# Performance work log

Measured on AMD Instinct MI355X. Metric: run time of the kernel, lower is better.

The kernel has to match this reference:

```python
import jax, jax.numpy as jnp
import numpy as np

B, S = 64, 512
VOCAB, DIM, FFDIM, NHEADS, BLOCKS = 512, 128, 512, 4, 4
MASK_INTER_CHOICES = False
LN_EPS = 1e-5
NEG = -1e30


def setup_inputs() -> dict:
    key = jax.random.key(0)
    ks = jax.random.split(key, 12)
    s = 0.02
    inp = dict(
        token_idxes=jax.random.randint(ks[0], (B, S), 0, VOCAB),
        n_pad_lefts=jax.random.randint(ks[1], (B,), 0, 9),
        cards_picked_n=jax.random.randint(ks[2], (B,), 1, 4),
        cards_skipped_n=jax.random.randint(ks[3], (B,), 1, 4),
        n_upgrades=jax.random.randint(ks[4], (B, S), 0, 3),
        emb=jax.random.normal(ks[5], (VOCAB, DIM), jnp.float32) * s,
        in_proj_w=jax.random.normal(ks[6], (BLOCKS, 3 * DIM, DIM), jnp.float32) * s,
        in_proj_b=jnp.zeros((BLOCKS, 3 * DIM), jnp.float32),
        out_w=jax.random.normal(ks[7], (BLOCKS, DIM, DIM), jnp.float32) * s,
        out_b=jnp.zeros((BLOCKS, DIM), jnp.float32),
        ln1_g=jnp.ones((BLOCKS, DIM), jnp.float32),
        ln1_b=jnp.zeros((BLOCKS, DIM), jnp.float32),
        ff1_w=jax.random.normal(ks[8], (BLOCKS, FFDIM, DIM), jnp.float32) * s,
        ff1_b=jnp.zeros((BLOCKS, FFDIM), jnp.float32),
        ff2_w=jax.random.normal(ks[9], (BLOCKS, DIM, FFDIM), jnp.float32) * s,
        ff2_b=jnp.zeros((BLOCKS, DIM), jnp.float32),
        ln2_g=jnp.ones((BLOCKS, DIM), jnp.float32),
        ln2_b=jnp.zeros((BLOCKS, DIM), jnp.float32),
        proj_w=jax.random.normal(ks[10], (2, DIM), jnp.float32) * s,
        proj_b=jnp.zeros((2,), jnp.float32),
    )
    return inp


def build_allowed(n_pad, n_choice):
    # allowed[b, i, j] == True where attention is permitted (torch mask==0)
    pos = jnp.arange(S)
    i = pos[None, :, None]
    j = pos[None, None, :]
    npd = n_pad[:, None, None]
    nc = n_choice[:, None, None]
    mid_i = (i >= npd) & (i < S - nc)
    mid_j = (j >= npd) & (j < S - nc)
    ch_i = i >= S - nc
    ch_j = j >= S - nc
    allowed = ((i < npd) & (i == j)) | (mid_i & mid_j) | (ch_i & mid_j)
    if MASK_INTER_CHOICES:
        allowed = allowed | (ch_i & (i == j))
    else:
        allowed = allowed | (ch_i & ch_j)
    return allowed  # [B, S, S]


def layernorm(x, g, b):
    m = jnp.mean(x, axis=-1, keepdims=True)
    v = jnp.var(x, axis=-1, keepdims=True)
    return (x - m) / jnp.sqrt(v + LN_EPS) * g + b


def mha_block(x, allowed, w_in, b_in, w_out, b_out, g1, b1, w1, bf1, w2, bf2, g2, b2):
    hd = DIM // NHEADS
    qkv = x @ w_in.T + b_in                       # [B,S,3D]
    q, k, v = jnp.split(qkv, 3, axis=-1)
    def heads(t):
        return t.reshape(x.shape[0], S, NHEADS, hd).transpose(0, 2, 1, 3)
    q, k, v = heads(q), heads(k), heads(v)
    scores = jnp.einsum('bhqd,bhkd->bhqk', q, k) / np.float32(np.sqrt(hd))
    scores = jnp.where(allowed[:, None, :, :], scores, NEG)
    attn = jax.nn.softmax(scores, axis=-1)
    o = jnp.einsum('bhqk,bhkd->bhqd', attn, v)
    o = o.transpose(0, 2, 1, 3).reshape(x.shape[0], S, DIM)
    o = o @ w_out.T + b_out
    x = layernorm(x + o, g1, b1)
    ff = jax.nn.relu(x @ w1.T + bf1) @ w2.T + bf2
    return layernorm(x + ff, g2, b2)


def reference(token_idxes, n_pad_lefts, cards_picked_n, cards_skipped_n, n_upgrades,
              emb, in_proj_w, in_proj_b, out_w, out_b, ln1_g, ln1_b,
              ff1_w, ff1_b, ff2_w, ff2_b, ln2_g, ln2_b, proj_w, proj_b):
    n_choice = cards_picked_n + cards_skipped_n
    feat = emb[token_idxes]                                   # [B,S,D]
    pos = jnp.arange(S)
    ch0 = (pos[None, :] >= n_choice[:, None]).astype(feat.dtype)
    feat = feat.at[:, :, 0].set(ch0)
    feat = feat.at[:, :, 1].set(jnp.clip(n_upgrades, 0, 1).astype(feat.dtype))
    allowed = build_allowed(n_pad_lefts, n_choice)
    for l in range(BLOCKS):
        feat = mha_block(feat, allowed, in_proj_w[l], in_proj_b[l], out_w[l], out_b[l],
                         ln1_g[l], ln1_b[l], ff1_w[l], ff1_b[l], ff2_w[l], ff2_b[l],
                         ln2_g[l], ln2_b[l])
    logits = feat @ proj_w.T + proj_b                          # [B,S,2]
    return jax.nn.softmax(logits, axis=2)
```

## Files before the change

kernel.cpp:

```cpp
#include <hip/hip_runtime.h>

#define CB   64
#define CS   512
#define CD   128
#define CH   4
#define CFF  512
#define CL   4
#define NEG_BIG -3.0e38f
#define SCALE 0.17677669529663687f
#define EXSC  0.25505654050961364f

typedef __attribute__((ext_vector_type(8))) short short8;
typedef __attribute__((ext_vector_type(4))) float f32x4;
typedef __attribute__((ext_vector_type(4))) unsigned int u32x4;

static __device__ __forceinline__ unsigned short f2b(float f) {
  union { float f; unsigned int u; } v; v.f = f;
  unsigned int u = v.u;
  unsigned int r = (u + 0x7fffu + ((u >> 16) & 1u)) >> 16;
  return (unsigned short)r;
}

__global__ void k_cvt_all(const float* __restrict__ inw, const float* __restrict__ outw,
                          const float* __restrict__ ffw1, const float* __restrict__ ffw2,
                          unsigned short* __restrict__ wq, unsigned short* __restrict__ wo,
                          unsigned short* __restrict__ w1, unsigned short* __restrict__ w2) {
  int bid = blockIdx.x;
  const float* src; unsigned short* dst; int base;
  if (bid < 192)      { src = inw;  dst = wq; base = bid; }
  else if (bid < 256) { src = outw; dst = wo; base = bid - 192; }
  else if (bid < 512) { src = ffw1; dst = w1; base = bid - 256; }
  else                { src = ffw2; dst = w2; base = bid - 512; }
  int i = base * 256 + threadIdx.x;
  float4 v = ((const float4*)src)[i];
  ((ushort4*)dst)[i] = make_ushort4(f2b(v.x), f2b(v.y), f2b(v.z), f2b(v.w));
}

__global__ void k_embed(const int* __restrict__ tok, const int* __restrict__ picked,
                        const int* __restrict__ skipped, const int* __restrict__ nupg,
                        const float* __restrict__ emb, float* __restrict__ featf,
                        unsigned short* __restrict__ featb) {
  int idx = blockIdx.x * 256 + threadIdx.x;
  int tp = idx >> 5, c4 = idx & 31;
  int t = tok[tp];
  float4 v = ((const float4*)emb)[t * 32 + c4];
  if (c4 == 0) {
    int b = tp >> 9, s = tp & 511;
    int nc = picked[b] + skipped[b];
    v.x = (s >= nc) ? 1.f : 0.f;
    v.y = (nupg[tp] > 0) ? 1.f : 0.f;
  }
  ((float4*)featf)[idx] = v;
  ((ushort4*)featb)[idx] = make_ushort4(f2b(v.x), f2b(v.y), f2b(v.z), f2b(v.w));
}

__global__ __launch_bounds__(256, 2) void k_gemm_qkv(
    const unsigned short* __restrict__ A, const unsigned short* __restrict__ W,
    const float* __restrict__ bias, unsigned short* __restrict__ qb,
    unsigned short* __restrict__ kb, unsigned short* __restrict__ vtb) {
  const int tid = threadIdx.x;
  const int m0 = blockIdx.x * 128;
  const int y = blockIdx.y;
  const int n0 = y * 128;
  const int lane = tid & 63, wid = tid >> 6;
  const int wm = wid >> 1, wn = wid & 1;
  const int lg = lane >> 4, r = lane & 15;

  f32x4 acc[4][4];
#pragma unroll
  for (int mi = 0; mi < 4; ++mi)
#pragma unroll
    for (int ni = 0; ni < 4; ++ni) acc[mi][ni] = (f32x4){0.f, 0.f, 0.f, 0.f};

  const unsigned short* Ab = A + (size_t)(m0 + wm * 64 + r) * 128 + lg * 8;
  const unsigned short* Wb = W + (size_t)(n0 + wn * 64 + r) * 128 + lg * 8;
#pragma unroll
  for (int kc = 0; kc < 4; ++kc) {
    short8 af[4], wf[4];
#pragma unroll
    for (int mi = 0; mi < 4; ++mi) af[mi] = *(const short8*)(Ab + mi * 2048 + kc * 32);
#pragma unroll
    for (int ni = 0; ni < 4; ++ni) wf[ni] = *(const short8*)(Wb + ni * 2048 + kc * 32);
#pragma unroll
    for (int mi = 0; mi < 4; ++mi)
#pragma unroll
      for (int ni = 0; ni < 4; ++ni)
        acc[mi][ni] = __builtin_amdgcn_mfma_f32_16x16x32_bf16(
            af[mi], wf[ni], acc[mi][ni], 0, 0, 0);
  }

  const int bidx = m0 >> 9;
  if (y < 2) {
    unsigned short* dst = y ? kb : qb;
    const float sc = y ? 1.f : EXSC;
#pragma unroll
    for (int mi = 0; mi < 4; ++mi)
#pragma unroll
      for (int ni = 0; ni < 4; ++ni) {
        int cl = wn * 64 + ni * 16 + r;
        int h = cl >> 5, dd = cl & 31;
        float bia = bias[n0 + cl];
        unsigned short* dp =
            dst + ((size_t)(bidx * 4 + h) * 512) * 32 + dd;
#pragma unroll
        for (int reg = 0; reg < 4; ++reg) {
          int s = (m0 + wm * 64 + mi * 16 + 4 * lg + reg) & 511;
          dp[(size_t)s * 32] = f2b((acc[mi][ni][reg] + bia) * sc);
        }
      }
  } else {
#pragma unroll
    for (int mi = 0; mi < 4; ++mi)
#pragma unroll
      for (int ni = 0; ni < 4; ++ni) {
        int cl = wn * 64 + ni * 16 + r;
        int h = cl >> 5, dd = cl & 31;
        float bia = bias[256 + cl];
        int s4 = (m0 + wm * 64 + mi * 16 + 4 * lg) & 511;
        int chunk = s4 >> 5, jl = s4 & 31;
        int p = 8 * ((jl & 15) >> 2) + 4 * (jl >> 4);
        ushort4 pk = make_ushort4(
            f2b(acc[mi][ni][0] + bia), f2b(acc[mi][ni][1] + bia),
            f2b(acc[mi][ni][2] + bia), f2b(acc[mi][ni][3] + bia));
        *(ushort4*)&vtb[((size_t)(bidx * 4 + h) * 32 + dd) * 512 + chunk * 32 + p] = pk;
      }
  }
}

__global__ __launch_bounds__(512, 1) void k_attn2(
    const unsigned short* __restrict__ qb, const unsigned short* __restrict__ kb,
    const unsigned short* __restrict__ vtb, const int* __restrict__ npadp,
    const int* __restrict__ picked, const int* __restrict__ skipped,
    unsigned short* __restrict__ obufb) {
  __shared__ __align__(16) unsigned short Ks[CS * 40];
  __shared__ __align__(16) unsigned short Vt[32 * CS];
  const int bh = blockIdx.x, b = bh >> 2, h = bh & 3;
  const int tid = threadIdx.x;
  const unsigned short* qbp = qb + ((size_t)bh * 512) * 32;
  const unsigned short* kbp = kb + ((size_t)bh * 512) * 32;
  const unsigned short* vtp = vtb + ((size_t)bh * 32) * 512;
#pragma unroll
  for (int i = 0; i < 4; ++i) {
    int f = tid + i * 512;
    int row = f >> 2, c = f & 3;
    *(uint4*)&Ks[row * 40 + c * 8] = *(const uint4*)(kbp + row * 32 + c * 8);
    int rowd = f >> 6, c16 = f & 63;
    *(uint4*)((char*)Vt + rowd * 1024 + ((c16 * 16) ^ ((rowd & 7) << 4))) =
        *(const uint4*)(vtp + rowd * 512 + c16 * 8);
  }
  const int lane = tid & 63, w = tid >> 6;
  const int lg = lane >> 4, r = lane & 15;
  const int npd = npadp[b];
  const int jhi_mid = CS - (picked[b] + skipped[b]);
  short8 onesf;
#pragma unroll
  for (int e = 0; e < 8; ++e) onesf[e] = (short)0x3F80;
  __syncthreads();

  short8 qf[4];
  int jhiR[4];
#pragma unroll
  for (int qt = 0; qt < 4; ++qt) {
    int q = w * 64 + qt * 16 + r;
    qf[qt] = *(const short8*)(qbp + (size_t)q * 32 + 8 * lg);
    jhiR[qt] = (q < jhi_mid) ? jhi_mid : CS;
  }
  f32x4 aO0[4], aO1[4], aL[4];
#pragma unroll
  for (int qt = 0; qt < 4; ++qt) {
    aO0[qt] = (f32x4){0.f, 0.f, 0.f, 0.f};
    aO1[qt] = (f32x4){0.f, 0.f, 0.f, 0.f};
    aL[qt]  = (f32x4){0.f, 0.f, 0.f, 0.f};
  }

  for (int jc = 0; jc < 16; ++jc) {
    const int j0 = jc * 32;
    short8 kf0 = *(const short8*)&Ks[(j0 + r) * 40 + 8 * lg];
    short8 kf1 = *(const short8*)&Ks[(j0 + 16 + r) * 40 + 8 * lg];
    const int jby = (j0 * 2 + 16 * lg) ^ ((r & 7) << 4);
    short8 vf0 = *(const short8*)((const char*)Vt + r * 1024 + jby);
    short8 vf1 = *(const short8*)((const char*)Vt + (16 + r) * 1024 + jby);
#pragma unroll
    for (int qt = 0; qt < 4; ++qt) {
      f32x4 z = (f32x4){0.f, 0.f, 0.f, 0.f};
      f32x4 s0 = __builtin_amdgcn_mfma_f32_16x16x32_bf16(kf0, qf[qt], z, 0, 0, 0);
      f32x4 s1 = __builtin_amdgcn_mfma_f32_16x16x32_bf16(kf1, qf[qt], z, 0, 0, 0);
      float p0[4], p1[4];
#pragma unroll
      for (int g = 0; g < 4; ++g) {
        p0[g] = exp2f(fminf(s0[g], 43.f));
        p1[g] = exp2f(fminf(s1[g], 43.f));
      }
      if (jc == 0) {
#pragma unroll
        for (int g = 0; g < 4; ++g)
          p0[g] = (4 * lg + g >= npd) ? p0[g] : 0.f;
      }
      if (jc == 15) {
#pragma unroll
        for (int g = 0; g < 4; ++g)
          p1[g] = (496 + 4 * lg + g < jhiR[qt]) ? p1[g] : 0.f;
      }
      unsigned int d0 = ((unsigned int)f2b(p0[1]) << 16) | f2b(p0[0]);
      unsigned int d1 = ((unsigned int)f2b(p0[3]) << 16) | f2b(p0[2]);
      unsigned int d2 = ((unsigned int)f2b(p1[1]) << 16) | f2b(p1[0]);
      unsigned int d3 = ((unsigned int)f2b(p1[3]) << 16) | f2b(p1[2]);
      u32x4 pd = (u32x4){d0, d1, d2, d3};
      short8 pa = __builtin_bit_cast(short8, pd);
      aL[qt]  = __builtin_amdgcn_mfma_f32_16x16x32_bf16(pa, onesf, aL[qt], 0, 0, 0);
      aO0[qt] = __builtin_amdgcn_mfma_f32_16x16x32_bf16(pa, vf0, aO0[qt], 0, 0, 0);
      aO1[qt] = __builtin_amdgcn_mfma_f32_16x16x32_bf16(pa, vf1, aO1[qt], 0, 0, 0);
    }
  }

#pragma unroll
  for (int qt = 0; qt < 4; ++qt)
#pragma unroll
    for (int g = 0; g < 4; ++g) {
      int qg = w * 64 + qt * 16 + 4 * lg + g;
      float inv = 1.f / aL[qt][g];
      unsigned short o0 = f2b(aO0[qt][g] * inv);
      unsigned short o1 = f2b(aO1[qt][g] * inv);
      if (qg < npd) {
        int p = 8 * (qg >> 2) + (qg & 3);
        o0 = *(const unsigned short*)((const char*)Vt + r * 1024 +
                                      ((2 * p) ^ ((r & 7) << 4)));
        o1 = *(const unsigned short*)((const char*)Vt + (16 + r) * 1024 +
                                      ((2 * p) ^ ((r & 7) << 4)));
      }
      unsigned short* op = obufb + ((size_t)(b * 512 + qg)) * 128 + h * 32;
      op[r] = o0;
      op[16 + r] = o1;
    }
}

__global__ __launch_bounds__(256, 2) void k_gemm_ln(
    const unsigned short* __restrict__ A, const unsigned short* __restrict__ W,
    const float* __restrict__ bias, float* __restrict__ outf,
    unsigned short* __restrict__ outb, const float* __restrict__ resf,
    const float* __restrict__ gam, const float* __restrict__ bet) {
  const int tid = threadIdx.x;
  const int m0 = blockIdx.x * 128;
  const int lane = tid & 63, wid = tid >> 6;
  const int wm = wid >> 1, wn = wid & 1;
  const int lg = lane >> 4, r = lane & 15;

  f32x4 acc[4][4];
#pragma unroll
  for (int mi = 0; mi < 4; ++mi)
#pragma unroll
    for (int ni = 0; ni < 4; ++ni) acc[mi][ni] = (f32x4){0.f, 0.f, 0.f, 0.f};

  const unsigned short* Ab = A + (size_t)(m0 + wm * 64 + r) * 128 + lg * 8;
  const unsigned short* Wb = W + (size_t)(wn * 64 + r) * 128 + lg * 8;
#pragma unroll
  for (int kc = 0; kc < 4; ++kc) {
    short8 af[4], wf[4];
#pragma unroll
    for (int mi = 0; mi < 4; ++mi) af[mi] = *(const short8*)(Ab + mi * 2048 + kc * 32);
#pragma unroll
    for (int ni = 0; ni < 4; ++ni) wf[ni] = *(const short8*)(Wb + ni * 2048 + kc * 32);
#pragma unroll
    for (int mi = 0; mi < 4; ++mi)
#pragma unroll
      for (int ni = 0; ni < 4; ++ni)
        acc[mi][ni] = __builtin_amdgcn_mfma_f32_16x16x32_bf16(
            af[mi], wf[ni], acc[mi][ni], 0, 0, 0);
  }

  __shared__ __align__(16) float Y[128 * 132];
#pragma unroll
  for (int mi = 0; mi < 4; ++mi)
#pragma unroll
    for (int ni = 0; ni < 4; ++ni) {
      int col = wn * 64 + ni * 16 + r;
      float bia = bias[col];
#pragma unroll
      for (int reg = 0; reg < 4; ++reg) {
        int row = wm * 64 + mi * 16 + 4 * lg + reg;
        Y[row * 132 + col] =
            acc[mi][ni][reg] + bia + resf[(size_t)(m0 + row) * 128 + col];
      }
    }
  __syncthreads();
  const int rr = tid >> 1, qq = tid & 1;
  float sum = 0.f, sum2 = 0.f;
  float4 yv[16];
#pragma unroll
  for (int c = 0; c < 16; ++c) {
    float4 y = *(const float4*)&Y[rr * 132 + qq * 64 + c * 4];
    yv[c] = y;
    sum += y.x + y.y + y.z + y.w;
    sum2 += y.x * y.x + y.y * y.y + y.z * y.z + y.w * y.w;
  }
  sum += __shfl_xor(sum, 1);
  sum2 += __shfl_xor(sum2, 1);
  const float mean = sum * (1.f / 128.f);
  const float var = sum2 * (1.f / 128.f) - mean * mean;
  const float rstd = rsqrtf(var + 1e-5f);
#pragma unroll
  for (int c = 0; c < 16; ++c) {
    float4 gv = ((const float4*)gam)[qq * 16 + c];
    float4 bv = ((const float4*)bet)[qq * 16 + c];
    float4 y = yv[c];
    y.x = (y.x - mean) * rstd * gv.x + bv.x;
    y.y = (y.y - mean) * rstd * gv.y + bv.y;
    y.z = (y.z - mean) * rstd * gv.z + bv.z;
    y.w = (y.w - mean) * rstd * gv.w + bv.w;
    ((float4*)outf)[(size_t)(m0 + rr) * 32 + qq * 16 + c] = y;
    *(ushort4*)&outb[(size_t)(m0 + rr) * 128 + qq * 64 + c * 4] =
        make_ushort4(f2b(y.x), f2b(y.y), f2b(y.z), f2b(y.w));
  }
}

__global__ __launch_bounds__(256, 2) void k_ffn_reg(
    const unsigned short* __restrict__ x, const unsigned short* __restrict__ w1b,
    const float* __restrict__ b1, const unsigned short* __restrict__ w2b,
    const float* __restrict__ b2, const float* __restrict__ gam,
    const float* __restrict__ bet, float* __restrict__ featf,
    unsigned short* __restrict__ featb) {
  __shared__ __align__(16) unsigned short hs[64 * 72];
  __shared__ __align__(16) float Y[64 * 132];
  const int tid = threadIdx.x;
  const int m0 = blockIdx.x * 64;
  const int lane = tid & 63, w = tid >> 6;
  const int wm = w >> 1, wn = w & 1;
  const int lg = lane >> 4, r = lane & 15;

  f32x4 accO[2][4];
#pragma unroll
  for (int mi = 0; mi < 2; ++mi)
#pragma unroll
    for (int ni = 0; ni < 4; ++ni) accO[mi][ni] = (f32x4){0.f, 0.f, 0.f, 0.f};

  const unsigned short* xb = x + (size_t)(m0 + wm * 32 + r) * 128 + lg * 8;
  const unsigned short* w2p = w2b + (size_t)(wn * 64 + r) * 512 + lg * 8;
  const unsigned short* hp = &hs[(wm * 32 + r) * 72 + lg * 8];

  for (int cc = 0; cc < 8; ++cc) {
    f32x4 accH[2][2];
#pragma unroll
    for (int mi = 0; mi < 2; ++mi)
#pragma unroll
      for (int ni = 0; ni < 2; ++ni) accH[mi][ni] = (f32x4){0.f, 0.f, 0.f, 0.f};
    const unsigned short* w1p =
        w1b + (size_t)(cc * 64 + wn * 32 + r) * 128 + lg * 8;
#pragma unroll
    for (int kc = 0; kc < 4; ++kc) {
      short8 af[2], wf[2];
#pragma unroll
      for (int mi = 0; mi < 2; ++mi) af[mi] = *(const short8*)(xb + mi * 2048 + kc * 32);
#pragma unroll
      for (int ni = 0; ni < 2; ++ni) wf[ni] = *(const short8*)(w1p + ni * 2048 + kc * 32);
#pragma unroll
      for (int mi = 0; mi < 2; ++mi)
#pragma unroll
        for (int ni = 0; ni < 2; ++ni)
          accH[mi][ni] = __builtin_amdgcn_mfma_f32_16x16x32_bf16(
              af[mi], wf[ni], accH[mi][ni], 0, 0, 0);
    }
    __syncthreads();
#pragma unroll
    for (int ni = 0; ni < 2; ++ni) {
      int n = wn * 32 + ni * 16 + r;
      float bv = b1[cc * 64 + n];
#pragma unroll
      for (int mi = 0; mi < 2; ++mi)
#pragma unroll
        for (int g = 0; g < 4; ++g) {
          int m = wm * 32 + mi * 16 + 4 * lg + g;
          hs[m * 72 + n] = f2b(fmaxf(accH[mi][ni][g] + bv, 0.f));
        }
    }
    __syncthreads();
#pragma unroll
    for (int kc2 = 0; kc2 < 2; ++kc2) {
      short8 af[2], wf[4];
#pragma unroll
      for (int mi = 0; mi < 2; ++mi) af[mi] = *(const short8*)(hp + mi * 1152 + kc2 * 32);
#pragma unroll
      for (int ni = 0; ni < 4; ++ni)
        wf[ni] = *(const short8*)(w2p + ni * 8192 + cc * 64 + kc2 * 32);
#pragma unroll
      for (int mi = 0; mi < 2; ++mi)
#pragma unroll
        for (int ni = 0; ni < 4; ++ni)
          accO[mi][ni] = __builtin_amdgcn_mfma_f32_16x16x32_bf16(
              af[mi], wf[ni], accO[mi][ni], 0, 0, 0);
    }
  }
#pragma unroll
  for (int mi = 0; mi < 2; ++mi)
#pragma unroll
    for (int ni = 0; ni < 4; ++ni) {
      int col = wn * 64 + ni * 16 + r;
      float bv = b2[col];
#pragma unroll
      for (int g = 0; g < 4; ++g) {
        int row = wm * 32 + mi * 16 + 4 * lg + g;
        Y[row * 132 + col] =
            accO[mi][ni][g] + bv + featf[(size_t)(m0 + row) * 128 + col];
      }
    }
  __syncthreads();
  const int rr = tid >> 2, qq = tid & 3;
  float sum = 0.f, sum2 = 0.f;
  float4 yv[8];
#pragma unroll
  for (int c = 0; c < 8; ++c) {
    float4 y = *(const float4*)&Y[rr * 132 + qq * 32 + c * 4];
    yv[c] = y;
    sum += y.x + y.y + y.z + y.w;
    sum2 += y.x * y.x + y.y * y.y + y.z * y.z + y.w * y.w;
  }
  sum += __shfl_xor(sum, 1); sum += __shfl_xor(sum, 2);
  sum2 += __shfl_xor(sum2, 1); sum2 += __shfl_xor(sum2, 2);
  const float mean = sum * (1.f / 128.f);
  const float var = sum2 * (1.f / 128.f) - mean * mean;
  const float rstd = rsqrtf(var + 1e-5f);
#pragma unroll
  for (int c = 0; c < 8; ++c) {
    float4 gv = ((const float4*)gam)[qq * 8 + c];
    float4 bv = ((const float4*)bet)[qq * 8 + c];
    float4 y = yv[c];
    y.x = (y.x - mean) * rstd * gv.x + bv.x;
    y.y = (y.y - mean) * rstd * gv.y + bv.y;
    y.z = (y.z - mean) * rstd * gv.z + bv.z;
    y.w = (y.w - mean) * rstd * gv.w + bv.w;
    ((float4*)featf)[(size_t)(m0 + rr) * 32 + qq * 8 + c] = y;
    *(ushort4*)&featb[(size_t)(m0 + rr) * 128 + qq * 32 + c * 4] =
        make_ushort4(f2b(y.x), f2b(y.y), f2b(y.z), f2b(y.w));
  }
}

__global__ void k_final(const float* __restrict__ feat, const float* __restrict__ pw,
                        const float* __restrict__ pb, float* __restrict__ out) {
  const int tid = threadIdx.x;
  const int tokb = blockIdx.x * 64 + (tid >> 2);
  const int qq = tid & 3;
  float d0 = 0.f, d1 = 0.f;
#pragma unroll
  for (int c = 0; c < 8; ++c) {
    float4 xv = ((const float4*)feat)[tokb * 32 + qq * 8 + c];
    float4 w0 = ((const float4*)pw)[qq * 8 + c];
    float4 w1 = ((const float4*)pw)[32 + qq * 8 + c];
    d0 += xv.x * w0.x + xv.y * w0.y + xv.z * w0.z + xv.w * w0.w;
    d1 += xv.x * w1.x + xv.y * w1.y + xv.z * w1.z + xv.w * w1.w;
  }
  d0 += __shfl_xor(d0, 1); d0 += __shfl_xor(d0, 2);
  d1 += __shfl_xor(d1, 1); d1 += __shfl_xor(d1, 2);
  if (qq == 0) {
    float l0 = d0 + pb[0], l1 = d1 + pb[1];
    float mx = fmaxf(l0, l1);
    float e0 = __expf(l0 - mx), e1 = __expf(l1 - mx);
    float inv = 1.f / (e0 + e1);
    ((float2*)out)[tokb] = make_float2(e0 * inv, e1 * inv);
  }
}

extern "C" void kernel_launch(void* const* d_in, const int* in_sizes, int n_in,
                              void* d_out, int out_size, void* d_ws, size_t ws_size,
                              hipStream_t stream) {
  const int* tok     = (const int*)d_in[0];
  const int* npad    = (const int*)d_in[1];
  const int* picked  = (const int*)d_in[2];
  const int* skipped = (const int*)d_in[3];
  const int* nupg    = (const int*)d_in[4];
  const float* emb   = (const float*)d_in[5];
  const float* inw   = (const float*)d_in[6];
  const float* inb   = (const float*)d_in[7];
  const float* outw  = (const float*)d_in[8];
  const float* outb_ = (const float*)d_in[9];
  const float* g1    = (const float*)d_in[10];
  const float* b1    = (const float*)d_in[11];
  const float* ffw1  = (const float*)d_in[12];
  const float* ffb1  = (const float*)d_in[13];
  const float* ffw2  = (const float*)d_in[14];
  const float* ffb2  = (const float*)d_in[15];
  const float* g2    = (const float*)d_in[16];
  const float* b2    = (const float*)d_in[17];
  const float* pw    = (const float*)d_in[18];
  const float* pb    = (const float*)d_in[19];

  char* wsb = (char*)d_ws;
  float*          featf = (float*)(wsb);
  unsigned short* qb    = (unsigned short*)(wsb + 16777216);
  unsigned short* kbuf  = (unsigned short*)(wsb + 25165824);
  unsigned short* vtb   = (unsigned short*)(wsb + 33554432);
  unsigned short* featb = (unsigned short*)(wsb + 41943040);
  unsigned short* obufb = (unsigned short*)(wsb + 50331648);
  unsigned short* wqkvb = (unsigned short*)(wsb + 58720256);
  unsigned short* woutb = (unsigned short*)(wsb + 59113472);
  unsigned short* wff1b = (unsigned short*)(wsb + 59244544);
  unsigned short* wff2b = (unsigned short*)(wsb + 59768832);

  k_cvt_all<<<dim3(768), 256, 0, stream>>>(inw, outw, ffw1, ffw2,
                                           wqkvb, woutb, wff1b, wff2b);

  k_embed<<<dim3(CB * CS * 32 / 256), 256, 0, stream>>>(
      tok, picked, skipped, nupg, emb, featf, featb);

  for (int l = 0; l < CL; ++l) {
    k_gemm_qkv<<<dim3(256, 3), 256, 0, stream>>>(
        featb, wqkvb + (size_t)l * 49152, inb + (size_t)l * 384, qb, kbuf, vtb);
    k_attn2<<<dim3(CB * CH), 512, 0, stream>>>(
        qb, kbuf, vtb, npad, picked, skipped, obufb);
    k_gemm_ln<<<dim3(256), 256, 0, stream>>>(
        obufb, woutb + (size_t)l * 16384, outb_ + (size_t)l * 128,
        featf, featb, featf, g1 + (size_t)l * 128, b1 + (size_t)l * 128);
    k_ffn_reg<<<dim3(512), 256, 0, stream>>>(
        featb, wff1b + (size_t)l * 65536, ffb1 + (size_t)l * 512,
        wff2b + (size_t)l * 65536, ffb2 + (size_t)l * 128,
        g2 + (size_t)l * 128, b2 + (size_t)l * 128, featf, featb);
  }

  k_final<<<dim3(CB * CS / 64), 256, 0, stream>>>(featf, pw, pb, (float*)d_out);
}
```

Before: 601.6 us.

## Keep FFN hidden activations in registers via transposed MFMA and permuted W2 layout

The FFN kernel is restructured so each wave owns 16 tokens and computes the hidden layer as W1·x^T. The MFMA output layout then maps directly onto the B-operand fragment for the second GEMM, so hidden activations are packed to bf16 in registers instead of going through shared memory with two barriers per chunk. The W2 weights are stored with a column permutation at conversion time so the packed register fragment lines up with the weight K ordering. The LayerNorm epilogue is done with cross-lane shuffles on the MFMA accumulator layout rather than a shared-memory staging tile. In exchange, each wave re-reads all of W1 and W2 from global/L2 for only 16 tokens, and the epilogue stores are narrow scalar writes.

```diff
diff --git a/kernel.cpp b/kernel.cpp
--- a/kernel.cpp
+++ b/kernel.cpp
@@ -26,14 +26,24 @@
                           unsigned short* __restrict__ wq, unsigned short* __restrict__ wo,
                           unsigned short* __restrict__ w1, unsigned short* __restrict__ w2) {
   int bid = blockIdx.x;
-  const float* src; unsigned short* dst; int base;
-  if (bid < 192)      { src = inw;  dst = wq; base = bid; }
-  else if (bid < 256) { src = outw; dst = wo; base = bid - 192; }
-  else if (bid < 512) { src = ffw1; dst = w1; base = bid - 256; }
-  else                { src = ffw2; dst = w2; base = bid - 512; }
-  int i = base * 256 + threadIdx.x;
-  float4 v = ((const float4*)src)[i];
-  ((ushort4*)dst)[i] = make_ushort4(f2b(v.x), f2b(v.y), f2b(v.z), f2b(v.w));
+  if (bid < 512) {
+    const float* src; unsigned short* dst; int base;
+    if (bid < 192)      { src = inw;  dst = wq; base = bid; }
+    else if (bid < 256) { src = outw; dst = wo; base = bid - 192; }
+    else                { src = ffw1; dst = w1; base = bid - 256; }
+    int i = base * 256 + threadIdx.x;
+    float4 v = ((const float4*)src)[i];
+    ((ushort4*)dst)[i] = make_ushort4(f2b(v.x), f2b(v.y), f2b(v.z), f2b(v.w));
+  } else {
+    int i = (bid - 512) * 256 + threadIdx.x;
+    int flat = i * 4;
+    int row = flat >> 9;
+    int n = flat & 511;
+    float4 v = ((const float4*)ffw2)[i];
+    int pos = (n & 480) + 8 * ((n & 15) >> 2) + 4 * ((n >> 4) & 1);
+    *(ushort4*)&w2[(size_t)row * 512 + pos] =
+        make_ushort4(f2b(v.x), f2b(v.y), f2b(v.z), f2b(v.w));
+  }
 }
 
 __global__ void k_embed(const int* __restrict__ tok, const int* __restrict__ picked,
@@ -313,123 +323,97 @@
   }
 }
 
-__global__ __launch_bounds__(256, 2) void k_ffn_reg(
+__global__ __launch_bounds__(256, 2) void k_ffn2(
     const unsigned short* __restrict__ x, const unsigned short* __restrict__ w1b,
-    const float* __restrict__ b1, const unsigned short* __restrict__ w2b,
+    const float* __restrict__ b1, const unsigned short* __restrict__ w2p,
     const float* __restrict__ b2, const float* __restrict__ gam,
     const float* __restrict__ bet, float* __restrict__ featf,
     unsigned short* __restrict__ featb) {
-  __shared__ __align__(16) unsigned short hs[64 * 72];
-  __shared__ __align__(16) float Y[64 * 132];
   const int tid = threadIdx.x;
-  const int m0 = blockIdx.x * 64;
   const int lane = tid & 63, w = tid >> 6;
-  const int wm = w >> 1, wn = w & 1;
   const int lg = lane >> 4, r = lane & 15;
-
-  f32x4 accO[2][4];
-#pragma unroll
-  for (int mi = 0; mi < 2; ++mi)
-#pragma unroll
-    for (int ni = 0; ni < 4; ++ni) accO[mi][ni] = (f32x4){0.f, 0.f, 0.f, 0.f};
-
-  const unsigned short* xb = x + (size_t)(m0 + wm * 32 + r) * 128 + lg * 8;
-  const unsigned short* w2p = w2b + (size_t)(wn * 64 + r) * 512 + lg * 8;
-  const unsigned short* hp = &hs[(wm * 32 + r) * 72 + lg * 8];
-
-  for (int cc = 0; cc < 8; ++cc) {
-    f32x4 accH[2][2];
-#pragma unroll
-    for (int mi = 0; mi < 2; ++mi)
-#pragma unroll
-      for (int ni = 0; ni < 2; ++ni) accH[mi][ni] = (f32x4){0.f, 0.f, 0.f, 0.f};
-    const unsigned short* w1p =
-        w1b + (size_t)(cc * 64 + wn * 32 + r) * 128 + lg * 8;
+  const int tokb = blockIdx.x * 64 + w * 16;
+
+  short8 xf[4];
+  const unsigned short* xp = x + (size_t)(tokb + r) * 128 + lg * 8;
+#pragma unroll
+  for (int kc = 0; kc < 4; ++kc) xf[kc] = *(const short8*)(xp + kc * 32);
+
+  f32x4 aO[8];
+#pragma unroll
+  for (int dt = 0; dt < 8; ++dt) aO[dt] = (f32x4){0.f, 0.f, 0.f, 0.f};
+
+  const unsigned short* w1base = w1b + (size_t)r * 128 + lg * 8;
+  const unsigned short* w2base = w2p + (size_t)r * 512 + lg * 8;
+
+#pragma unroll
+  for (int c = 0; c < 16; ++c) {
+    f32x4 hA = (f32x4){0.f, 0.f, 0.f, 0.f};
+    f32x4 hB = (f32x4){0.f, 0.f, 0.f, 0.f};
 #pragma unroll
     for (int kc = 0; kc < 4; ++kc) {
-      short8 af[2], wf[2];
-#pragma unroll
-      for (int mi = 0; mi < 2; ++mi) af[mi] = *(const short8*)(xb + mi * 2048 + kc * 32);
-#pragma unroll
-      for (int ni = 0; ni < 2; ++ni) wf[ni] = *(const short8*)(w1p + ni * 2048 + kc * 32);
-#pragma unroll
-      for (int mi = 0; mi < 2; ++mi)
-#pragma unroll
-        for (int ni = 0; ni < 2; ++ni)
-          accH[mi][ni] = __builtin_amdgcn_mfma_f32_16x16x32_bf16(
-              af[mi], wf[ni], accH[mi][ni], 0, 0, 0);
-    }
-    __syncthreads();
-#pragma unroll
-    for (int ni = 0; ni < 2; ++ni) {
-      int n = wn * 32 + ni * 16 + r;
-      float bv = b1[cc * 64 + n];
-#pragma unroll
-      for (int mi = 0; mi < 2; ++mi)
-#pragma unroll
-        for (int g = 0; g < 4; ++g) {
-          int m = wm * 32 + mi * 16 + 4 * lg + g;
-          hs[m * 72 + n] = f2b(fmaxf(accH[mi][ni][g] + bv, 0.f));
-        }
-    }
-    __syncthreads();
-#pragma unroll
-    for (int kc2 = 0; kc2 < 2; ++kc2) {
-      short8 af[2], wf[4];
-#pragma unroll
-      for (int mi = 0; mi < 2; ++mi) af[mi] = *(const short8*)(hp + mi * 1152 + kc2 * 32);
-#pragma unroll
-      for (int ni = 0; ni < 4; ++ni)
-        wf[ni] = *(const short8*)(w2p + ni * 8192 + cc * 64 + kc2 * 32);
-#pragma unroll
-      for (int mi = 0; mi < 2; ++mi)
-#pragma unroll
-        for (int ni = 0; ni < 4; ++ni)
-          accO[mi][ni] = __builtin_amdgcn_mfma_f32_16x16x32_bf16(
-              af[mi], wf[ni], accO[mi][ni], 0, 0, 0);
-    }
-  }
-#pragma unroll
-  for (int mi = 0; mi < 2; ++mi)
-#pragma unroll
-    for (int ni = 0; ni < 4; ++ni) {
-      int col = wn * 64 + ni * 16 + r;
-      float bv = b2[col];
-#pragma unroll
-      for (int g = 0; g < 4; ++g) {
-        int row = wm * 32 + mi * 16 + 4 * lg + g;
-        Y[row * 132 + col] =
-            accO[mi][ni][g] + bv + featf[(size_t)(m0 + row) * 128 + col];
-      }
-    }
-  __syncthreads();
-  const int rr = tid >> 2, qq = tid & 3;
-  float sum = 0.f, sum2 = 0.f;
-  float4 yv[8];
-#pragma unroll
-  for (int c = 0; c < 8; ++c) {
-    float4 y = *(const float4*)&Y[rr * 132 + qq * 32 + c * 4];
-    yv[c] = y;
-    sum += y.x + y.y + y.z + y.w;
-    sum2 += y.x * y.x + y.y * y.y + y.z * y.z + y.w * y.w;
-  }
-  sum += __shfl_xor(sum, 1); sum += __shfl_xor(sum, 2);
-  sum2 += __shfl_xor(sum2, 1); sum2 += __shfl_xor(sum2, 2);
-  const float mean = sum * (1.f / 128.f);
-  const float var = sum2 * (1.f / 128.f) - mean * mean;
-  const float rstd = rsqrtf(var + 1e-5f);
-#pragma unroll
-  for (int c = 0; c < 8; ++c) {
-    float4 gv = ((const float4*)gam)[qq * 8 + c];
-    float4 bv = ((const float4*)bet)[qq * 8 + c];
-    float4 y = yv[c];
-    y.x = (y.x - mean) * rstd * gv.x + bv.x;
-    y.y = (y.y - mean) * rstd * gv.y + bv.y;
-    y.z = (y.z - mean) * rstd * gv.z + bv.z;
-    y.w = (y.w - mean) * rstd * gv.w + bv.w;
-    ((float4*)featf)[(size_t)(m0 + rr) * 32 + qq * 8 + c] = y;
-    *(ushort4*)&featb[(size_t)(m0 + rr) * 128 + qq * 32 + c * 4] =
-        make_ushort4(f2b(y.x), f2b(y.y), f2b(y.z), f2b(y.w));
+      short8 wA = *(const short8*)(w1base + (size_t)(32 * c) * 128 + kc * 32);
+      short8 wB = *(const short8*)(w1base + (size_t)(32 * c + 16) * 128 + kc * 32);
+      hA = __builtin_amdgcn_mfma_f32_16x16x32_bf16(wA, xf[kc], hA, 0, 0, 0);
+      hB = __builtin_amdgcn_mfma_f32_16x16x32_bf16(wB, xf[kc], hB, 0, 0, 0);
+    }
+    float pA[4], pB[4];
+#pragma unroll
+    for (int g = 0; g < 4; ++g) {
+      pA[g] = fmaxf(hA[g] + b1[32 * c + 4 * lg + g], 0.f);
+      pB[g] = fmaxf(hB[g] + b1[32 * c + 16 + 4 * lg + g], 0.f);
+    }
+    unsigned int d0 = ((unsigned int)f2b(pA[1]) << 16) | f2b(pA[0]);
+    unsigned int d1 = ((unsigned int)f2b(pA[3]) << 16) | f2b(pA[2]);
+    unsigned int d2 = ((unsigned int)f2b(pB[1]) << 16) | f2b(pB[0]);
+    unsigned int d3 = ((unsigned int)f2b(pB[3]) << 16) | f2b(pB[2]);
+    u32x4 pd = (u32x4){d0, d1, d2, d3};
+    short8 pa = __builtin_bit_cast(short8, pd);
+#pragma unroll
+    for (int dt = 0; dt < 8; ++dt) {
+      short8 w2f = *(const short8*)(w2base + (size_t)(dt * 16) * 512 + c * 32);
+      aO[dt] = __builtin_amdgcn_mfma_f32_16x16x32_bf16(pa, w2f, aO[dt], 0, 0, 0);
+    }
+  }
+
+  float b2v[8], gv[8], bv[8];
+#pragma unroll
+  for (int dt = 0; dt < 8; ++dt) {
+    b2v[dt] = b2[r + 16 * dt];
+    gv[dt]  = gam[r + 16 * dt];
+    bv[dt]  = bet[r + 16 * dt];
+  }
+  float yv[8][4];
+  float s1[4] = {0.f, 0.f, 0.f, 0.f}, s2[4] = {0.f, 0.f, 0.f, 0.f};
+#pragma unroll
+  for (int g = 0; g < 4; ++g) {
+    const float* fp = featf + (size_t)(tokb + 4 * lg + g) * 128 + r;
+#pragma unroll
+    for (int dt = 0; dt < 8; ++dt) {
+      float t = aO[dt][g] + b2v[dt] + fp[16 * dt];
+      yv[dt][g] = t;
+      s1[g] += t;
+      s2[g] += t * t;
+    }
+  }
+#pragma unroll
+  for (int g = 0; g < 4; ++g) {
+#pragma unroll
+    for (int d = 1; d < 16; d <<= 1) {
+      s1[g] += __shfl_xor(s1[g], d);
+      s2[g] += __shfl_xor(s2[g], d);
+    }
+    const float mean = s1[g] * (1.f / 128.f);
+    const float var = s2[g] * (1.f / 128.f) - mean * mean;
+    const float rstd = rsqrtf(var + 1e-5f);
+    float* fo = featf + (size_t)(tokb + 4 * lg + g) * 128 + r;
+    unsigned short* bo = featb + (size_t)(tokb + 4 * lg + g) * 128 + r;
+#pragma unroll
+    for (int dt = 0; dt < 8; ++dt) {
+      float yy = (yv[dt][g] - mean) * rstd * gv[dt] + bv[dt];
+      fo[16 * dt] = yy;
+      bo[16 * dt] = f2b(yy);
+    }
   }
 }
 
@@ -492,10 +476,10 @@
   unsigned short* wqkvb = (unsigned short*)(wsb + 58720256);
   unsigned short* woutb = (unsigned short*)(wsb + 59113472);
   unsigned short* wff1b = (unsigned short*)(wsb + 59244544);
-  unsigned short* wff2b = (unsigned short*)(wsb + 59768832);
+  unsigned short* wff2p = (unsigned short*)(wsb + 59768832);
 
   k_cvt_all<<<dim3(768), 256, 0, stream>>>(inw, outw, ffw1, ffw2,
-                                           wqkvb, woutb, wff1b, wff2b);
+                                           wqkvb, woutb, wff1b, wff2p);
 
   k_embed<<<dim3(CB * CS * 32 / 256), 256, 0, stream>>>(
       tok, picked, skipped, nupg, emb, featf, featb);
@@ -508,9 +492,9 @@
     k_gemm_ln<<<dim3(256), 256, 0, stream>>>(
         obufb, woutb + (size_t)l * 16384, outb_ + (size_t)l * 128,
         featf, featb, featf, g1 + (size_t)l * 128, b1 + (size_t)l * 128);
-    k_ffn_reg<<<dim3(512), 256, 0, stream>>>(
+    k_ffn2<<<dim3(512), 256, 0, stream>>>(
         featb, wff1b + (size_t)l * 65536, ffb1 + (size_t)l * 512,
-        wff2b + (size_t)l * 65536, ffb2 + (size_t)l * 128,
+        wff2p + (size_t)l * 65536, ffb2 + (size_t)l * 128,
         g2 + (size_t)l * 128, b2 + (size_t)l * 128, featf, featb);
   }
 
```

Result: slower. 684.0 us (+13.7%).
